# Optimization experiments

Hardware: AMD Instinct MI355X
Metric: run time of the kernel (lower is better)

## Reference

```python
import jax, jax.numpy as jnp
import numpy as np

N_NODES = 100000
N_EDGES = 1600000
N_GRAPHS = 256
IN_FEATS = 64
H_FEATS = 128
GN_EPS = 1e-5


def setup_inputs() -> dict:
    key = jax.random.key(0)
    ks = jax.random.split(key, 8)
    inputs = jax.random.normal(ks[0], (N_NODES, IN_FEATS), dtype=jnp.float32)
    edge_index = jax.random.randint(ks[1], (2, N_EDGES), 0, N_NODES, dtype=jnp.int64)
    batch = jnp.sort(jax.random.randint(ks[2], (N_NODES,), 0, N_GRAPHS, dtype=jnp.int64))
    edge_attr = jax.random.normal(ks[3], (N_EDGES, 8), dtype=jnp.float32)
    W1 = jax.random.normal(ks[4], (IN_FEATS, H_FEATS), dtype=jnp.float32) * 0.05
    W2 = jax.random.normal(ks[5], (H_FEATS, H_FEATS), dtype=jnp.float32) * 0.05
    W3 = jax.random.normal(ks[6], (H_FEATS, H_FEATS), dtype=jnp.float32) * 0.05
    return {
        'inputs': inputs, 'edge_index': edge_index, 'batch': batch, 'edge_attr': edge_attr,
        'W1': W1, 'b1': jnp.zeros((H_FEATS,), jnp.float32),
        'W2': W2, 'b2': jnp.zeros((H_FEATS,), jnp.float32),
        'W3': W3, 'b3': jnp.zeros((H_FEATS,), jnp.float32),
        'gn_weight': jnp.ones((H_FEATS,), jnp.float32),
        'gn_bias': jnp.zeros((H_FEATS,), jnp.float32),
        'gn_mean_scale': jnp.ones((H_FEATS,), jnp.float32),
    }


def reference(inputs, edge_index, batch, edge_attr, W1, b1, W2, b2, W3, b3, gn_weight, gn_bias, gn_mean_scale):
    src, dst = edge_index[0], edge_index[1]
    # GINConv with eps=0: h_i = MLP((1+eps)*x_i + sum_{j in N(i)} x_j)
    agg = jax.ops.segment_sum(inputs[src], dst, num_segments=N_NODES)
    h = inputs + agg
    # 3-layer ReLU MLP
    h = jax.nn.relu(h @ W1 + b1)
    h = jax.nn.relu(h @ W2 + b2)
    h = jax.nn.relu(h @ W3 + b3)
    # GraphNorm (per-graph mean shift with learnable mean_scale, then per-graph rms normalize)
    cnt = jnp.maximum(jax.ops.segment_sum(jnp.ones((N_NODES, 1), h.dtype), batch, num_segments=N_GRAPHS), 1.0)
    mean = jax.ops.segment_sum(h, batch, num_segments=N_GRAPHS) / cnt  # [G, H]
    out = h - mean[batch] * gn_mean_scale
    var = jax.ops.segment_sum(out * out, batch, num_segments=N_GRAPHS) / cnt  # [G, H]
    h_emb = out / jnp.sqrt(var[batch] + GN_EPS) * gn_weight + gn_bias
    # add_residue=False -> plain ReLU
    h_emb = jax.nn.relu(h_emb)
    # global max pool over each graph segment
    flat = jax.ops.segment_max(h_emb, batch, num_segments=N_GRAPHS)
    return (h_emb, flat, edge_index, edge_attr, batch)
```

## Files before the change

### kernel.cpp

```cpp
#include <hip/hip_runtime.h>
#include <math.h>

#define N_NODES 100000
#define N_EDGES 1600000
#define N_GRAPHS 256
#define IN_F 64
#define H_F 128
#define GN_EPS 1e-5f
#define PAD 32
#define NBINS 8
#define LCAP 512
#define BINCAP (1 << 18)
#define NSUB 16
#define SUBW 782
#define SBCAP 16384

typedef __attribute__((ext_vector_type(8))) short bf16x8;
typedef __attribute__((ext_vector_type(4))) float f32x4;

__device__ __forceinline__ float bf2f(unsigned short u) {
  return __uint_as_float(((unsigned int)u) << 16);
}
__device__ __forceinline__ unsigned short f2bf(float f) {
  unsigned int u = __float_as_uint(f);
  u += 0x7FFFu + ((u >> 16) & 1u);
  return (unsigned short)(u >> 16);
}
__device__ __forceinline__ int bsearch_batch(const int* __restrict__ batch, int target) {
  int lo = 0, hi = N_NODES;
  while (lo < hi) { int mid = (lo + hi) >> 1; if (batch[mid] < target) lo = mid + 1; else hi = mid; }
  return lo;
}

#define PREP_XH   1600000
#define PREP_GS   (PREP_XH + 16384)
#define PREP_WT   (PREP_GS + 40960)
#define PREP_CTR  (PREP_WT + 40)
#define PREP_FL   (PREP_CTR + 8192)
__global__ __launch_bounds__(256) void k_prep(
    const float4* __restrict__ xin, const float* __restrict__ W1,
    const float* __restrict__ W2, const float* __restrict__ W3,
    ushort4* __restrict__ xh4, float4* __restrict__ gsum4,
    unsigned short* __restrict__ wt, int4* __restrict__ ctr4,
    float4* __restrict__ flat4) {
  int i = blockIdx.x * 256 + threadIdx.x;
  if (i < PREP_XH) {
    float4 v = xin[i];
    ushort4 o;
    o.x = f2bf(v.x); o.y = f2bf(v.y); o.z = f2bf(v.z); o.w = f2bf(v.w);
    xh4[i] = o;
  } else if (i < PREP_GS) {
    gsum4[i - PREP_XH] = make_float4(0.f, 0.f, 0.f, 0.f);
  } else if (i < PREP_WT) {
    int j = i - PREP_GS;
    if (j < 8192) {
      int n = j >> 6, k = j & 63;
      wt[j] = f2bf(W1[(size_t)k * H_F + n]);
    } else if (j < 24576) {
      int jj = j - 8192;
      int n = jj >> 7, k = jj & 127;
      wt[j] = f2bf(W2[(size_t)k * H_F + n]);
    } else {
      int jj = j - 24576;
      int n = jj >> 7, k = jj & 127;
      wt[j] = f2bf(W3[(size_t)k * H_F + n]);
    }
  } else if (i < PREP_CTR) {
    ctr4[i - PREP_WT] = make_int4(0, 0, 0, 0);
  } else if (i < PREP_FL) {
    flat4[i - PREP_CTR] = make_float4(-INFINITY, -INFINITY, -INFINITY, -INFINITY);
  }
}

__global__ __launch_bounds__(256) void k_bin(
    const int* __restrict__ src, const int* __restrict__ dst,
    unsigned int* __restrict__ binBuf, int* __restrict__ gbc) {
  __shared__ unsigned int ebuf[NBINS][LCAP];
  __shared__ int lcnt[NBINS];
  __shared__ int lbase[NBINS];
  const int t = threadIdx.x;
  if (t < NBINS) lcnt[t] = 0;
  __syncthreads();
  for (int e0 = blockIdx.x * 256; e0 < N_EDGES; e0 += gridDim.x * 256) {
    int e = e0 + t;
    if (e < N_EDGES) {
      int s = src[e], d = dst[e];
      int b = d / 12500;
      int p = atomicAdd(&lcnt[b], 1);
      ebuf[b][p] = ((unsigned)(d - b * 12500) << 17) | (unsigned)s;
    }
    __syncthreads();
    if (t < NBINS && lcnt[t] >= 256) lbase[t] = atomicAdd(&gbc[t], lcnt[t]);
    __syncthreads();
#pragma unroll
    for (int b = 0; b < NBINS; ++b) {
      int c = lcnt[b];
      if (c >= 256) {
        unsigned int* gp = binBuf + (size_t)b * BINCAP + lbase[b];
        for (int i = t; i < c; i += 256) gp[i] = ebuf[b][i];
      }
    }
    __syncthreads();
    if (t < NBINS && lcnt[t] >= 256) lcnt[t] = 0;
    __syncthreads();
  }
  if (t < NBINS && lcnt[t] > 0) lbase[t] = atomicAdd(&gbc[t], lcnt[t]);
  __syncthreads();
#pragma unroll
  for (int b = 0; b < NBINS; ++b) {
    int c = lcnt[b];
    if (c > 0) {
      unsigned int* gp = binBuf + (size_t)b * BINCAP + lbase[b];
      for (int i = t; i < c; i += 256) gp[i] = ebuf[b][i];
    }
  }
}

__global__ __launch_bounds__(256) void k_bin2(
    const unsigned int* __restrict__ binBuf, const int* __restrict__ gbc,
    unsigned int* __restrict__ binBuf2, int* __restrict__ gbc2) {
  __shared__ unsigned int ebuf[NSUB][LCAP];
  __shared__ int lcnt[NSUB];
  __shared__ int lbase[NSUB];
  const int t = threadIdx.x;
  const int p = blockIdx.x & 7;
  const int blk = blockIdx.x >> 3;
  const int nb = gbc[p];
  const unsigned int* buf = binBuf + (size_t)p * BINCAP;
  if (t < NSUB) lcnt[t] = 0;
  __syncthreads();
  for (int i0 = blk * 256; i0 < nb; i0 += 32 * 256) {
    int i = i0 + t;
    if (i < nb) {
      unsigned int e = buf[i];
      int dloc = (int)(e >> 17);
      int sub = dloc / SUBW;
      int p2 = atomicAdd(&lcnt[sub], 1);
      ebuf[sub][p2] = ((unsigned)(dloc - sub * SUBW) << 17) | (e & 131071u);
    }
    __syncthreads();
    if (t < NSUB && lcnt[t] >= 256)
      lbase[t] = atomicAdd(&gbc2[p * NSUB + t], lcnt[t]);
    __syncthreads();
#pragma unroll
    for (int b = 0; b < NSUB; ++b) {
      int c = lcnt[b];
      if (c >= 256) {
        unsigned int* gp = binBuf2 + (size_t)(p * NSUB + b) * SBCAP + lbase[b];
        for (int i2 = t; i2 < c; i2 += 256) gp[i2] = ebuf[b][i2];
      }
    }
    __syncthreads();
    if (t < NSUB && lcnt[t] >= 256) lcnt[t] = 0;
    __syncthreads();
  }
  if (t < NSUB && lcnt[t] > 0)
    lbase[t] = atomicAdd(&gbc2[p * NSUB + t], lcnt[t]);
  __syncthreads();
#pragma unroll
  for (int b = 0; b < NSUB; ++b) {
    int c = lcnt[b];
    if (c > 0) {
      unsigned int* gp = binBuf2 + (size_t)(p * NSUB + b) * SBCAP + lbase[b];
      for (int i2 = t; i2 < c; i2 += 256) gp[i2] = ebuf[b][i2];
    }
  }
}

__global__ __launch_bounds__(256) void k_fill5(
    const unsigned int* __restrict__ binBuf2, const int* __restrict__ gbc2,
    int* __restrict__ csr, int* __restrict__ cnt,
    int* __restrict__ ovfc, int* __restrict__ ovf) {
  __shared__ int lcsr[SUBW * PAD];
  __shared__ int lcnt[SUBW];
  const int t = threadIdx.x;
  const int p = blockIdx.x & 7;
  const int sub = blockIdx.x >> 3;
  for (int j = t; j < SUBW; j += 256) lcnt[j] = 0;
  __syncthreads();
  const int n2 = gbc2[p * NSUB + sub];
  const unsigned int* buf = binBuf2 + (size_t)(p * NSUB + sub) * SBCAP;
  const int dbase = p * 12500 + sub * SUBW;
  for (int i = t; i < n2; i += 256) {
    unsigned int e = buf[i];
    int dloc2 = (int)(e >> 17);
    int s = (int)(e & 131071u);
    int pos = atomicAdd(&lcnt[dloc2], 1);
    if (pos < PAD) {
      lcsr[dloc2 * PAD + pos] = s;
    } else {
      int o = atomicAdd(ovfc, 1);
      ovf[2 * o] = s;
      ovf[2 * o + 1] = dbase + dloc2;
    }
  }
  __syncthreads();
  int rows = 12500 - sub * SUBW; if (rows > SUBW) rows = SUBW;
  int total4 = rows * (PAD / 4);
  int4* dst4 = (int4*)(csr + (size_t)dbase * PAD);
  const int4* src4 = (const int4*)lcsr;
  for (int i = t; i < total4; i += 256) dst4[i] = src4[i];
  for (int j = t; j < rows; j += 256)
    cnt[dbase + j] = lcnt[j];
}

__global__ __launch_bounds__(256) void k_gather(
    const unsigned short* __restrict__ xh, const int* __restrict__ csr,
    const int* __restrict__ cnt, unsigned short* __restrict__ xa,
    const int* __restrict__ ovfc, const int* __restrict__ ovf) {
  int wid = (blockIdx.x * 256 + threadIdx.x) >> 6;
  if (wid >= N_NODES) return;
  const int lane = threadIdx.x & 63;
  const int g = lane >> 4;
  const int fl = lane & 15;
  int rawdeg = cnt[wid];
  int deg = rawdeg > PAD ? PAD : rawdeg;
  int myE = csr[(size_t)wid * PAD + (lane & 31)];
  float s0 = 0.f, s1 = 0.f, s2 = 0.f, s3 = 0.f;
  int j = g;
  for (; j + 12 < deg; j += 16) {
    int sA = __shfl(myE, j);
    int sB = __shfl(myE, j + 4);
    int sC = __shfl(myE, j + 8);
    int sD = __shfl(myE, j + 12);
    ushort4 a = *(const ushort4*)&xh[(size_t)sA * IN_F + fl * 4];
    ushort4 b = *(const ushort4*)&xh[(size_t)sB * IN_F + fl * 4];
    ushort4 c = *(const ushort4*)&xh[(size_t)sC * IN_F + fl * 4];
    ushort4 d = *(const ushort4*)&xh[(size_t)sD * IN_F + fl * 4];
    s0 += bf2f(a.x) + bf2f(b.x) + bf2f(c.x) + bf2f(d.x);
    s1 += bf2f(a.y) + bf2f(b.y) + bf2f(c.y) + bf2f(d.y);
    s2 += bf2f(a.z) + bf2f(b.z) + bf2f(c.z) + bf2f(d.z);
    s3 += bf2f(a.w) + bf2f(b.w) + bf2f(c.w) + bf2f(d.w);
  }
  for (; j < deg; j += 4) {
    int sA = __shfl(myE, j);
    ushort4 a = *(const ushort4*)&xh[(size_t)sA * IN_F + fl * 4];
    s0 += bf2f(a.x); s1 += bf2f(a.y); s2 += bf2f(a.z); s3 += bf2f(a.w);
  }
  if (rawdeg > PAD && g == 0) {
    int n = *ovfc;
    for (int o = 0; o < n; ++o) {
      if (ovf[2 * o + 1] == wid) {
        int s = ovf[2 * o];
        ushort4 a = *(const ushort4*)&xh[(size_t)s * IN_F + fl * 4];
        s0 += bf2f(a.x); s1 += bf2f(a.y); s2 += bf2f(a.z); s3 += bf2f(a.w);
      }
    }
  }
  s0 += __shfl_xor(s0, 16); s1 += __shfl_xor(s1, 16);
  s2 += __shfl_xor(s2, 16); s3 += __shfl_xor(s3, 16);
  s0 += __shfl_xor(s0, 32); s1 += __shfl_xor(s1, 32);
  s2 += __shfl_xor(s2, 32); s3 += __shfl_xor(s3, 32);
  if (g == 0) {
    ushort4 self = *(const ushort4*)&xh[(size_t)wid * IN_F + fl * 4];
    s0 += bf2f(self.x); s1 += bf2f(self.y);
    s2 += bf2f(self.z); s3 += bf2f(self.w);
    ushort4 r;
    r.x = f2bf(s0); r.y = f2bf(s1); r.z = f2bf(s2); r.w = f2bf(s3);
    *(ushort4*)&xa[(size_t)wid * IN_F + fl * 4] = r;
  }
}

__global__ __launch_bounds__(512) void k_mlp(
    const unsigned short* __restrict__ xa,
    const unsigned short* __restrict__ wt1,
    const unsigned short* __restrict__ wt2,
    const unsigned short* __restrict__ wt3,
    const float* __restrict__ b1, const float* __restrict__ b2,
    const float* __restrict__ b3,
    unsigned short* __restrict__ h3,
    const int* __restrict__ batch,
    float* __restrict__ gsum, float* __restrict__ gsumq) {
  __shared__ unsigned short sh[128 * 128];
  __shared__ float ssum[H_F], ssq[H_F];
  const int t = threadIdx.x;
  const int lane = t & 63;
  const int wv = t >> 6;
  const int row16 = lane & 15;
  const int kg = lane >> 4;
  const long blk0 = (long)blockIdx.x * 128;
  const int lr0 = (wv & 3) * 32;
  const int nb = (wv >> 2) * 4;
  f32x4 acc0[4], acc1[4];

  {
    long arow0 = blk0 + lr0 + row16;      if (arow0 > N_NODES - 1) arow0 = N_NODES - 1;
    long arow1 = blk0 + lr0 + 16 + row16; if (arow1 > N_NODES - 1) arow1 = N_NODES - 1;
    bf16x8 a0[2], a1[2];
    const unsigned short* ap0 = xa + arow0 * IN_F + kg * 8;
    const unsigned short* ap1 = xa + arow1 * IN_F + kg * 8;
#pragma unroll
    for (int s = 0; s < 2; ++s) {
      a0[s] = *(const bf16x8*)(ap0 + s * 32);
      a1[s] = *(const bf16x8*)(ap1 + s * 32);
    }
#pragma unroll
    for (int n = 0; n < 4; ++n) {
      acc0[n] = (f32x4){0.f, 0.f, 0.f, 0.f};
      acc1[n] = (f32x4){0.f, 0.f, 0.f, 0.f};
    }
#pragma unroll
    for (int n = 0; n < 4; ++n) {
      const unsigned short* wpn =
          wt1 + (size_t)((nb + n) * 16 + row16) * IN_F + kg * 8;
      bf16x8 b[2];
      b[0] = *(const bf16x8*)(wpn);
      b[1] = *(const bf16x8*)(wpn + 32);
      acc0[n] = __builtin_amdgcn_mfma_f32_16x16x32_bf16(a0[0], b[0], acc0[n], 0, 0, 0);
      acc0[n] = __builtin_amdgcn_mfma_f32_16x16x32_bf16(a0[1], b[1], acc0[n], 0, 0, 0);
      acc1[n] = __builtin_amdgcn_mfma_f32_16x16x32_bf16(a1[0], b[0], acc1[n], 0, 0, 0);
      acc1[n] = __builtin_amdgcn_mfma_f32_16x16x32_bf16(a1[1], b[1], acc1[n], 0, 0, 0);
    }
#pragma unroll
    for (int n = 0; n < 4; ++n) {
      int col = (nb + n) * 16 + row16;
      float bv = b1[col];
#pragma unroll
      for (int r = 0; r < 4; ++r) {
        int lrow0 = lr0 + kg * 4 + r;
        int lrow1 = lrow0 + 16;
        sh[lrow0 * 128 + (col ^ ((lrow0 & 7) << 3))] = f2bf(fmaxf(acc0[n][r] + bv, 0.f));
        sh[lrow1 * 128 + (col ^ ((lrow1 & 7) << 3))] = f2bf(fmaxf(acc1[n][r] + bv, 0.f));
      }
    }
  }
  __syncthreads();

  {
    const int lA0 = lr0 + row16, lA1 = lr0 + 16 + row16;
    bf16x8 a0[4], a1[4];
#pragma unroll
    for (int s = 0; s < 4; ++s) {
      int K0 = s * 32 + kg * 8;
      a0[s] = *(const bf16x8*)&sh[lA0 * 128 + (K0 ^ ((lA0 & 7) << 3))];
      a1[s] = *(const bf16x8*)&sh[lA1 * 128 + (K0 ^ ((lA1 & 7) << 3))];
    }
#pragma unroll
    for (int n = 0; n < 4; ++n) {
      acc0[n] = (f32x4){0.f, 0.f, 0.f, 0.f};
      acc1[n] = (f32x4){0.f, 0.f, 0.f, 0.f};
    }
#pragma unroll
    for (int n = 0; n < 4; ++n) {
      const unsigned short* wpn =
          wt2 + (size_t)((nb + n) * 16 + row16) * H_F + kg * 8;
      bf16x8 b[4];
#pragma unroll
      for (int s = 0; s < 4; ++s) b[s] = *(const bf16x8*)(wpn + s * 32);
#pragma unroll
      for (int s = 0; s < 4; ++s) {
        acc0[n] = __builtin_amdgcn_mfma_f32_16x16x32_bf16(a0[s], b[s], acc0[n], 0, 0, 0);
        acc1[n] = __builtin_amdgcn_mfma_f32_16x16x32_bf16(a1[s], b[s], acc1[n], 0, 0, 0);
      }
    }
    __syncthreads();
#pragma unroll
    for (int n = 0; n < 4; ++n) {
      int col = (nb + n) * 16 + row16;
      float bv = b2[col];
#pragma unroll
      for (int r = 0; r < 4; ++r) {
        int lrow0 = lr0 + kg * 4 + r;
        int lrow1 = lrow0 + 16;
        sh[lrow0 * 128 + (col ^ ((lrow0 & 7) << 3))] = f2bf(fmaxf(acc0[n][r] + bv, 0.f));
        sh[lrow1 * 128 + (col ^ ((lrow1 & 7) << 3))] = f2bf(fmaxf(acc1[n][r] + bv, 0.f));
      }
    }
  }
  __syncthreads();

  {
    const int lA0 = lr0 + row16, lA1 = lr0 + 16 + row16;
    bf16x8 a0[4], a1[4];
#pragma unroll
    for (int s = 0; s < 4; ++s) {
      int K0 = s * 32 + kg * 8;
      a0[s] = *(const bf16x8*)&sh[lA0 * 128 + (K0 ^ ((lA0 & 7) << 3))];
      a1[s] = *(const bf16x8*)&sh[lA1 * 128 + (K0 ^ ((lA1 & 7) << 3))];
    }
#pragma unroll
    for (int n = 0; n < 4; ++n) {
      acc0[n] = (f32x4){0.f, 0.f, 0.f, 0.f};
      acc1[n] = (f32x4){0.f, 0.f, 0.f, 0.f};
    }
#pragma unroll
    for (int n = 0; n < 4; ++n) {
      const unsigned short* wpn =
          wt3 + (size_t)((nb + n) * 16 + row16) * H_F + kg * 8;
      bf16x8 b[4];
#pragma unroll
      for (int s = 0; s < 4; ++s) b[s] = *(const bf16x8*)(wpn + s * 32);
#pragma unroll
      for (int s = 0; s < 4; ++s) {
        acc0[n] = __builtin_amdgcn_mfma_f32_16x16x32_bf16(a0[s], b[s], acc0[n], 0, 0, 0);
        acc1[n] = __builtin_amdgcn_mfma_f32_16x16x32_bf16(a1[s], b[s], acc1[n], 0, 0, 0);
      }
    }
#pragma unroll
    for (int n = 0; n < 4; ++n) {
      int col = (nb + n) * 16 + row16;
      float bv = b3[col];
#pragma unroll
      for (int r = 0; r < 4; ++r) {
        long row0 = blk0 + lr0 + kg * 4 + r;
        long row1 = row0 + 16;
        if (row0 < N_NODES)
          h3[row0 * H_F + col] = f2bf(fmaxf(acc0[n][r] + bv, 0.f));
        if (row1 < N_NODES)
          h3[row1 * H_F + col] = f2bf(fmaxf(acc1[n][r] + bv, 0.f));
      }
    }
    long lastrow = blk0 + 127; if (lastrow > N_NODES - 1) lastrow = N_NODES - 1;
    const int glo = batch[blk0];
    const int ghi = batch[lastrow];
    int br0[4], br1[4];
#pragma unroll
    for (int r = 0; r < 4; ++r) {
      long row0 = blk0 + lr0 + kg * 4 + r;
      long row1 = row0 + 16;
      br0[r] = (row0 < N_NODES) ? batch[row0] : -1;
      br1[r] = (row1 < N_NODES) ? batch[row1] : -1;
    }
    for (int g = glo; g <= ghi; ++g) {
      if (t < H_F) { ssum[t] = 0.f; ssq[t] = 0.f; }
      __syncthreads();
#pragma unroll
      for (int n = 0; n < 4; ++n) {
        int col = (nb + n) * 16 + row16;
        float bvn = b3[col];
        float sn = 0.f, qn = 0.f;
#pragma unroll
        for (int r = 0; r < 4; ++r) {
          if (br0[r] == g) { float f = fmaxf(acc0[n][r] + bvn, 0.f); sn += f; qn += f * f; }
          if (br1[r] == g) { float f = fmaxf(acc1[n][r] + bvn, 0.f); sn += f; qn += f * f; }
        }
        sn += __shfl_xor(sn, 16); qn += __shfl_xor(qn, 16);
        sn += __shfl_xor(sn, 32); qn += __shfl_xor(qn, 32);
        if (kg == 0) {
          atomicAdd(&ssum[col], sn);
          atomicAdd(&ssq[col], qn);
        }
      }
      __syncthreads();
      if (t < H_F) {
        unsafeAtomicAdd(&gsum[(size_t)g * H_F + t], ssum[t]);
        unsafeAtomicAdd(&gsumq[(size_t)g * H_F + t], ssq[t]);
      }
      __syncthreads();
    }
  }
}

__global__ __launch_bounds__(256) void k_apply2(
    const unsigned short* __restrict__ h3, const int* __restrict__ batch,
    const float* __restrict__ gsum, const float* __restrict__ gsumsq,
    const float* __restrict__ gms, const float* __restrict__ gw,
    const float* __restrict__ gb, float* __restrict__ hemb,
    float* __restrict__ flat) {
  const int t = threadIdx.x;
  const int rg = t >> 5, fq = t & 31;
  const int m0 = blockIdx.x * 32;
  const int r0 = m0 + rg * 4;
  const int c0 = fq * 4;
  const float4 bb = *(const float4*)&gb[c0];
  const float4 gm = *(const float4*)&gms[c0];
  const float4 gwv = *(const float4*)&gw[c0];
  const int glo = batch[m0], ghi = batch[m0 + 31];
  __shared__ int sb[2];
  __shared__ __align__(16) float4 mred[8][32];
  if (glo == ghi) {
    if (t < 2) sb[t] = bsearch_batch(batch, glo + t);
    __syncthreads();
    float c = fmaxf((float)(sb[1] - sb[0]), 1.0f);
    float4 S = *(const float4*)&gsum[(size_t)glo * H_F + c0];
    float4 Q = *(const float4*)&gsumsq[(size_t)glo * H_F + c0];
    float4 mm, ss;
    {
      float mean, ms, var;
      mean = S.x / c; ms = mean * gm.x; var = fmaxf(Q.x / c - 2.f * ms * mean + ms * ms, 0.f);
      mm.x = ms; ss.x = gwv.x * rsqrtf(var + GN_EPS);
      mean = S.y / c; ms = mean * gm.y; var = fmaxf(Q.y / c - 2.f * ms * mean + ms * ms, 0.f);
      mm.y = ms; ss.y = gwv.y * rsqrtf(var + GN_EPS);
      mean = S.z / c; ms = mean * gm.z; var = fmaxf(Q.z / c - 2.f * ms * mean + ms * ms, 0.f);
      mm.z = ms; ss.z = gwv.z * rsqrtf(var + GN_EPS);
      mean = S.w / c; ms = mean * gm.w; var = fmaxf(Q.w / c - 2.f * ms * mean + ms * ms, 0.f);
      mm.w = ms; ss.w = gwv.w * rsqrtf(var + GN_EPS);
    }
    float4 mx = {-INFINITY, -INFINITY, -INFINITY, -INFINITY};
#pragma unroll
    for (int i = 0; i < 4; ++i) {
      size_t idx = (size_t)(r0 + i) * H_F + c0;
      ushort4 u = *(const ushort4*)&h3[idx];
      float4 v;
      v.x = fmaxf((bf2f(u.x) - mm.x) * ss.x + bb.x, 0.f);
      v.y = fmaxf((bf2f(u.y) - mm.y) * ss.y + bb.y, 0.f);
      v.z = fmaxf((bf2f(u.z) - mm.z) * ss.z + bb.z, 0.f);
      v.w = fmaxf((bf2f(u.w) - mm.w) * ss.w + bb.w, 0.f);
      *(float4*)&hemb[idx] = v;
      mx.x = fmaxf(mx.x, v.x); mx.y = fmaxf(mx.y, v.y);
      mx.z = fmaxf(mx.z, v.z); mx.w = fmaxf(mx.w, v.w);
    }
    mred[rg][fq] = mx;
    __syncthreads();
    if (rg == 0) {
#pragma unroll
      for (int j = 1; j < 8; ++j) {
        float4 a = mred[j][fq];
        mx.x = fmaxf(mx.x, a.x); mx.y = fmaxf(mx.y, a.y);
        mx.z = fmaxf(mx.z, a.z); mx.w = fmaxf(mx.w, a.w);
      }
      int* pf = (int*)&flat[(size_t)glo * H_F + c0];
      atomicMax(pf + 0, __float_as_int(mx.x));
      atomicMax(pf + 1, __float_as_int(mx.y));
      atomicMax(pf + 2, __float_as_int(mx.z));
      atomicMax(pf + 3, __float_as_int(mx.w));
    }
  } else {
    int gcur = -1;
    float4 mm = {0,0,0,0}, ss = {0,0,0,0};
    float4 mx = {-INFINITY, -INFINITY, -INFINITY, -INFINITY};
#pragma unroll
    for (int i = 0; i < 4; ++i) {
      int g = batch[r0 + i];
      if (g != gcur) {
        if (gcur >= 0) {
          int* pf = (int*)&flat[(size_t)gcur * H_F + c0];
          atomicMax(pf + 0, __float_as_int(mx.x));
          atomicMax(pf + 1, __float_as_int(mx.y));
          atomicMax(pf + 2, __float_as_int(mx.z));
          atomicMax(pf + 3, __float_as_int(mx.w));
          mx = make_float4(-INFINITY, -INFINITY, -INFINITY, -INFINITY);
        }
        gcur = g;
        int lo = bsearch_batch(batch, g);
        int hi = bsearch_batch(batch, g + 1);
        float c = fmaxf((float)(hi - lo), 1.0f);
        float4 S = *(const float4*)&gsum[(size_t)g * H_F + c0];
        float4 Q = *(const float4*)&gsumsq[(size_t)g * H_F + c0];
        float mean, ms, var;
        mean = S.x / c; ms = mean * gm.x; var = fmaxf(Q.x / c - 2.f * ms * mean + ms * ms, 0.f);
        mm.x = ms; ss.x = gwv.x * rsqrtf(var + GN_EPS);
        mean = S.y / c; ms = mean * gm.y; var = fmaxf(Q.y / c - 2.f * ms * mean + ms * ms, 0.f);
        mm.y = ms; ss.y = gwv.y * rsqrtf(var + GN_EPS);
        mean = S.z / c; ms = mean * gm.z; var = fmaxf(Q.z / c - 2.f * ms * mean + ms * ms, 0.f);
        mm.z = ms; ss.z = gwv.z * rsqrtf(var + GN_EPS);
        mean = S.w / c; ms = mean * gm.w; var = fmaxf(Q.w / c - 2.f * ms * mean + ms * ms, 0.f);
        mm.w = ms; ss.w = gwv.w * rsqrtf(var + GN_EPS);
      }
      size_t idx = (size_t)(r0 + i) * H_F + c0;
      ushort4 u = *(const ushort4*)&h3[idx];
      float4 v;
      v.x = fmaxf((bf2f(u.x) - mm.x) * ss.x + bb.x, 0.f);
      v.y = fmaxf((bf2f(u.y) - mm.y) * ss.y + bb.y, 0.f);
      v.z = fmaxf((bf2f(u.z) - mm.z) * ss.z + bb.z, 0.f);
      v.w = fmaxf((bf2f(u.w) - mm.w) * ss.w + bb.w, 0.f);
      *(float4*)&hemb[idx] = v;
      mx.x = fmaxf(mx.x, v.x); mx.y = fmaxf(mx.y, v.y);
      mx.z = fmaxf(mx.z, v.z); mx.w = fmaxf(mx.w, v.w);
    }
    int* pf = (int*)&flat[(size_t)gcur * H_F + c0];
    atomicMax(pf + 0, __float_as_int(mx.x));
    atomicMax(pf + 1, __float_as_int(mx.y));
    atomicMax(pf + 2, __float_as_int(mx.z));
    atomicMax(pf + 3, __float_as_int(mx.w));
  }
}

#define CP_EI  800000
#define CP_EA  (CP_EI + 3200000)
#define CP_B   (CP_EA + 25000)
__global__ __launch_bounds__(256) void k_copyall(
    const int4* __restrict__ ei4, const float4* __restrict__ ea4,
    const int4* __restrict__ b4, float4* __restrict__ o_ei4,
    float4* __restrict__ o_ea4, float4* __restrict__ o_b4) {
  int i = blockIdx.x * 256 + threadIdx.x;
  if (i < CP_EI) {
    int4 v = ei4[i];
    o_ei4[i] = make_float4((float)v.x, (float)v.y, (float)v.z, (float)v.w);
  } else if (i < CP_EA) {
    int j = i - CP_EI;
    o_ea4[j] = ea4[j];
  } else if (i < CP_B) {
    int j = i - CP_EA;
    int4 v = b4[j];
    o_b4[j] = make_float4((float)v.x, (float)v.y, (float)v.z, (float)v.w);
  }
}

extern "C" void kernel_launch(void* const* d_in, const int* in_sizes, int n_in,
                              void* d_out, int out_size, void* d_ws, size_t ws_size,
                              hipStream_t stream) {
  const float* inputs = (const float*)d_in[0];
  const int*   ei     = (const int*)d_in[1];
  const int*   batch  = (const int*)d_in[2];
  const float* eattr  = (const float*)d_in[3];
  const float* W1 = (const float*)d_in[4];
  const float* b1 = (const float*)d_in[5];
  const float* W2 = (const float*)d_in[6];
  const float* b2 = (const float*)d_in[7];
  const float* W3 = (const float*)d_in[8];
  const float* b3 = (const float*)d_in[9];
  const float* gw  = (const float*)d_in[10];
  const float* gb  = (const float*)d_in[11];
  const float* gms = (const float*)d_in[12];

  float* out = (float*)d_out;
  float* hemb  = out;
  float* flat  = out + 12800000;
  float* o_ei  = out + 12832768;
  float* o_ea  = out + 16032768;
  float* o_b   = out + 28832768;

  unsigned int*   binBuf  = (unsigned int*)hemb;
  unsigned int*   binBuf2 = (unsigned int*)(hemb + 2100000);
  unsigned short* xh = (unsigned short*)(hemb + 4200000);
  unsigned short* xa = (unsigned short*)(hemb + 7600000);
  int*            csr = (int*)o_ea;
  unsigned short* h3  = (unsigned short*)(o_ea + 6400000);
  int*   cnt   = (int*)o_ei;
  int*   ovfc  = (int*)o_ei + 100000;
  int*   gbc   = (int*)o_ei + 100008;
  int*   gbc2  = (int*)o_ei + 100016;
  int*   ovf   = (int*)o_ei + 100160;
  float* gsum  = o_ei + 200000;
  float* gsumq = o_ei + 232768;
  unsigned short* wt  = (unsigned short*)(o_ei + 350000);
  unsigned short* wt1 = wt;
  unsigned short* wt2 = wt + 8192;
  unsigned short* wt3 = wt + 24576;

  k_prep<<<(PREP_FL + 255) / 256, 256, 0, stream>>>(
      (const float4*)inputs, W1, W2, W3, (ushort4*)xh, (float4*)gsum, wt,
      (int4*)ovfc, (float4*)flat);
  k_bin<<<512, 256, 0, stream>>>(ei, ei + N_EDGES, binBuf, gbc);
  k_bin2<<<256, 256, 0, stream>>>(binBuf, gbc, binBuf2, gbc2);
  k_fill5<<<NBINS * NSUB, 256, 0, stream>>>(binBuf2, gbc2, csr, cnt, ovfc, ovf);
  k_gather<<<(N_NODES * 64 + 255) / 256, 256, 0, stream>>>(xh, csr, cnt, xa, ovfc, ovf);
  const int mg = (N_NODES + 127) / 128;
  k_mlp<<<mg, 512, 0, stream>>>(xa, wt1, wt2, wt3, b1, b2, b3, h3, batch, gsum, gsumq);
  k_apply2<<<N_NODES / 32, 256, 0, stream>>>(h3, batch, gsum, gsumq, gms, gw, gb,
                                             hemb, flat);
  k_copyall<<<(CP_B + 255) / 256, 256, 0, stream>>>(
      (const int4*)ei, (const float4*)eattr, (const int4*)batch,
      (float4*)o_ei, (float4*)o_ea, (float4*)o_b);
}
```

Before: 247.2 us.

## Fuse edge_index and batch conversion copies into spare MLP kernel blocks

```diff
diff --git a/kernel.cpp b/kernel.cpp
--- a/kernel.cpp
+++ b/kernel.cpp
@@ -14,6 +14,10 @@
 #define NSUB 16
 #define SUBW 782
 #define SBCAP 16384
+#define MG 782
+#define CPB 1612
+#define CP_EI4 800000
+#define CP_TOT 825000
 
 typedef __attribute__((ext_vector_type(8))) short bf16x8;
 typedef __attribute__((ext_vector_type(4))) float f32x4;
@@ -270,10 +274,26 @@
     const float* __restrict__ b3,
     unsigned short* __restrict__ h3,
     const int* __restrict__ batch,
-    float* __restrict__ gsum, float* __restrict__ gsumq) {
+    float* __restrict__ gsum, float* __restrict__ gsumq,
+    const int4* __restrict__ ei4, const int4* __restrict__ bat4,
+    float4* __restrict__ o_ei4, float4* __restrict__ o_b4) {
   __shared__ unsigned short sh[128 * 128];
   __shared__ float ssum[H_F], ssq[H_F];
   const int t = threadIdx.x;
+  if (blockIdx.x >= MG) {
+    int cb = blockIdx.x - MG;
+    for (int i = cb * 512 + t; i < CP_TOT; i += CPB * 512) {
+      if (i < CP_EI4) {
+        int4 v = ei4[i];
+        o_ei4[i] = make_float4((float)v.x, (float)v.y, (float)v.z, (float)v.w);
+      } else {
+        int j = i - CP_EI4;
+        int4 v = bat4[j];
+        o_b4[j] = make_float4((float)v.x, (float)v.y, (float)v.z, (float)v.w);
+      }
+    }
+    return;
+  }
   const int lane = t & 63;
   const int wv = t >> 6;
   const int row16 = lane & 15;
@@ -566,25 +586,10 @@
   }
 }
 
-#define CP_EI  800000
-#define CP_EA  (CP_EI + 3200000)
-#define CP_B   (CP_EA + 25000)
-__global__ __launch_bounds__(256) void k_copyall(
-    const int4* __restrict__ ei4, const float4* __restrict__ ea4,
-    const int4* __restrict__ b4, float4* __restrict__ o_ei4,
-    float4* __restrict__ o_ea4, float4* __restrict__ o_b4) {
+__global__ __launch_bounds__(256) void k_copy_ea(
+    const float4* __restrict__ ea4, float4* __restrict__ o_ea4, int n4) {
   int i = blockIdx.x * 256 + threadIdx.x;
-  if (i < CP_EI) {
-    int4 v = ei4[i];
-    o_ei4[i] = make_float4((float)v.x, (float)v.y, (float)v.z, (float)v.w);
-  } else if (i < CP_EA) {
-    int j = i - CP_EI;
-    o_ea4[j] = ea4[j];
-  } else if (i < CP_B) {
-    int j = i - CP_EA;
-    int4 v = b4[j];
-    o_b4[j] = make_float4((float)v.x, (float)v.y, (float)v.z, (float)v.w);
-  }
+  if (i < n4) o_ea4[i] = ea4[i];
 }
 
 extern "C" void kernel_launch(void* const* d_in, const int* in_sizes, int n_in,
@@ -617,17 +622,17 @@
   unsigned short* xa = (unsigned short*)(hemb + 7600000);
   int*            csr = (int*)o_ea;
   unsigned short* h3  = (unsigned short*)(o_ea + 6400000);
+  float* gsum  = o_ea + 3200000;
+  float* gsumq = o_ea + 3232768;
+  unsigned short* wt  = (unsigned short*)(o_ea + 3265536);
+  unsigned short* wt1 = wt;
+  unsigned short* wt2 = wt + 8192;
+  unsigned short* wt3 = wt + 24576;
   int*   cnt   = (int*)o_ei;
   int*   ovfc  = (int*)o_ei + 100000;
   int*   gbc   = (int*)o_ei + 100008;
   int*   gbc2  = (int*)o_ei + 100016;
   int*   ovf   = (int*)o_ei + 100160;
-  float* gsum  = o_ei + 200000;
-  float* gsumq = o_ei + 232768;
-  unsigned short* wt  = (unsigned short*)(o_ei + 350000);
-  unsigned short* wt1 = wt;
-  unsigned short* wt2 = wt + 8192;
-  unsigned short* wt3 = wt + 24576;
 
   k_prep<<<(PREP_FL + 255) / 256, 256, 0, stream>>>(
       (const float4*)inputs, W1, W2, W3, (ushort4*)xh, (float4*)gsum, wt,
@@ -636,11 +641,12 @@
   k_bin2<<<256, 256, 0, stream>>>(binBuf, gbc, binBuf2, gbc2);
   k_fill5<<<NBINS * NSUB, 256, 0, stream>>>(binBuf2, gbc2, csr, cnt, ovfc, ovf);
   k_gather<<<(N_NODES * 64 + 255) / 256, 256, 0, stream>>>(xh, csr, cnt, xa, ovfc, ovf);
-  const int mg = (N_NODES + 127) / 128;
-  k_mlp<<<mg, 512, 0, stream>>>(xa, wt1, wt2, wt3, b1, b2, b3, h3, batch, gsum, gsumq);
+  k_mlp<<<MG + CPB, 512, 0, stream>>>(xa, wt1, wt2, wt3, b1, b2, b3, h3, batch,
+                                      gsum, gsumq, (const int4*)ei,
+                                      (const int4*)batch, (float4*)o_ei,
+                                      (float4*)o_b);
   k_apply2<<<N_NODES / 32, 256, 0, stream>>>(h3, batch, gsum, gsumq, gms, gw, gb,
                                              hemb, flat);
-  k_copyall<<<(CP_B + 255) / 256, 256, 0, stream>>>(
-      (const int4*)ei, (const float4*)eattr, (const int4*)batch,
-      (float4*)o_ei, (float4*)o_ea, (float4*)o_b);
-}
+  k_copy_ea<<<(N_EDGES * 2 + 255) / 256, 256, 0, stream>>>(
+      (const float4*)eattr, (float4*)o_ea, N_EDGES * 2);
+}
```

New measurement: 245.4 us. About the same (-0.7%).
